# Performance work log

Hardware: AMD Instinct MI355X
Metric: run time of the kernel (lower is better)

The kernel has to match this reference:

```python
import jax, jax.numpy as jnp
import numpy as np

T = 35            # cfg.VOXEL_POINT_COUNT
D, H, W = 10, 400, 352  # cfg.INPUT_DEPTH/HEIGHT/WIDTH
EPS = 1e-5


def _vfe(x, mask, w, b, gamma, beta):
    # x: [K, T, Cin]; mask: [K, T, 1]
    h = jax.nn.relu(jnp.einsum('ktc,cu->ktu', x, w) + b)        # [K, T, U]
    mean = jnp.mean(h, axis=(0, 1))
    var = jnp.var(h, axis=(0, 1))
    h = (h - mean) * jax.lax.rsqrt(var + EPS) * gamma + beta    # batch-stat BN
    agg = jnp.max(h, axis=1, keepdims=True)                     # [K, 1, U]
    cat = jnp.concatenate([h, jnp.broadcast_to(agg, h.shape)], axis=-1)  # [K, T, 2U]
    return cat * mask


def setup_inputs() -> dict:
    key = jax.random.key(0)
    ks = jax.random.split(key, 12)
    K = 40000
    feature = jax.random.normal(ks[0], (K, T, 7), dtype=jnp.float32)
    # zero out ~half the points so the nonzero mask is meaningful
    keep = jax.random.bernoulli(ks[1], 0.5, (K, T, 1)).astype(jnp.float32)
    feature = feature * keep
    bidx = jax.random.randint(ks[2], (K, 1), 0, 2)
    didx = jax.random.randint(ks[3], (K, 1), 0, D)
    hidx = jax.random.randint(ks[4], (K, 1), 0, H)
    widx = jax.random.randint(ks[5], (K, 1), 0, W)
    coordinate = jnp.concatenate([bidx, didx, hidx, widx], axis=1).astype(jnp.int32)
    s = 0.1
    return {
        'feature': feature,
        'w1': jax.random.normal(ks[6], (7, 16), dtype=jnp.float32) * s,
        'b1': jnp.zeros((16,), dtype=jnp.float32),
        'gamma1': jnp.ones((16,), dtype=jnp.float32),
        'beta1': jnp.zeros((16,), dtype=jnp.float32),
        'w2': jax.random.normal(ks[7], (32, 32), dtype=jnp.float32) * s,
        'b2': jnp.zeros((32,), dtype=jnp.float32),
        'gamma2': jnp.ones((32,), dtype=jnp.float32),
        'beta2': jnp.zeros((32,), dtype=jnp.float32),
        'coordinate': coordinate,
        'batch_size': 2,
    }


def reference(feature, w1, b1, gamma1, beta1, w2, b2, gamma2, beta2, coordinate, batch_size):
    # mask: voxel point is valid if any channel nonzero (max over channels != 0)
    mask = (jnp.max(feature, axis=2, keepdims=True) != 0).astype(feature.dtype)  # [K, T, 1]
    x = _vfe(feature, mask, w1, b1, gamma1, beta1)   # [K, T, 32]
    x = _vfe(x, mask, w2, b2, gamma2, beta2)         # [K, T, 64]
    voxelwise = jnp.max(x, axis=1)                   # [K, 64]
    out = jnp.zeros((batch_size, D, H, W, 64), dtype=voxelwise.dtype)
    out = out.at[coordinate[:, 0], coordinate[:, 1], coordinate[:, 2], coordinate[:, 3]].add(voxelwise)
    return out
```

## Files before the change

kernel.cpp:

```cpp
#include <hip/hip_runtime.h>
#include <math.h>

#define TT 35
#define DD 10
#define HD 400
#define WD 352
#define CIN 7
#define U1 16
#define U2 32
#define EPSV 1e-5f

#define WS_A1 0
#define WS_B1 16
#define WS_A2 32
#define WS_B2 64
#define WS_SUM1 256
#define WS_SSQ1 768
#define WS_SUM2 1280
#define WS_SSQ2 3328
#define NC1 32
#define NC2 64
#define WS_ZERO_FLOATS 5376

__global__ __launch_bounds__(256) void k_stats1(
    const float* __restrict__ feat, const float* __restrict__ w1,
    const float* __restrict__ b1, float* __restrict__ ws, int P) {
  __shared__ float s_w1[CIN * U1];
  __shared__ float s_b1[U1];
  __shared__ float s_red[4][2 * U1];

  int tid = threadIdx.x;
  if (tid < CIN * U1) s_w1[tid] = w1[tid];
  if (tid < U1) s_b1[tid] = b1[tid];
  __syncthreads();

  float sum[U1], ssq[U1];
#pragma unroll
  for (int u = 0; u < U1; ++u) { sum[u] = 0.f; ssq[u] = 0.f; }

  int stride = gridDim.x * blockDim.x;
  for (int p = blockIdx.x * blockDim.x + tid; p < P; p += stride) {
    const float* f = feat + (size_t)p * CIN;
    float x[CIN];
#pragma unroll
    for (int c = 0; c < CIN; ++c) x[c] = f[c];
#pragma unroll
    for (int u = 0; u < U1; ++u) {
      float acc = s_b1[u];
#pragma unroll
      for (int c = 0; c < CIN; ++c) acc += x[c] * s_w1[c * U1 + u];
      float h = fmaxf(acc, 0.f);
      sum[u] += h;
      ssq[u] += h * h;
    }
  }

  int lane = tid & 63, wv = tid >> 6;
#pragma unroll
  for (int u = 0; u < U1; ++u) {
    float s = sum[u], q = ssq[u];
    for (int off = 32; off; off >>= 1) {
      s += __shfl_down(s, off);
      q += __shfl_down(q, off);
    }
    if (lane == 0) { s_red[wv][u] = s; s_red[wv][U1 + u] = q; }
  }
  __syncthreads();
  if (tid < 2 * U1) {
    float tot = s_red[0][tid] + s_red[1][tid] + s_red[2][tid] + s_red[3][tid];
    int copy = blockIdx.x & (NC1 - 1);
    int u = tid & (U1 - 1);
    int base = (tid < U1) ? WS_SUM1 : WS_SSQ1;
    atomicAdd(&ws[base + copy * U1 + u], tot);
  }
}

__global__ void k_fin1(const float* __restrict__ gamma,
                       const float* __restrict__ beta, float* __restrict__ ws,
                       float invN) {
  int u = threadIdx.x;
  float s = 0.f, q = 0.f;
  for (int c = 0; c < NC1; ++c) {
    s += ws[WS_SUM1 + c * U1 + u];
    q += ws[WS_SSQ1 + c * U1 + u];
  }
  float mean = s * invN;
  float var = q * invN - mean * mean;
  float istd = 1.0f / sqrtf(var + EPSV);
  float A = gamma[u] * istd;
  ws[WS_A1 + u] = A;
  ws[WS_B1 + u] = beta[u] - mean * A;
}

__global__ void k_fin2(const float* __restrict__ gamma,
                       const float* __restrict__ beta, float* __restrict__ ws,
                       float invN) {
  int u = threadIdx.x;
  float s = 0.f, q = 0.f;
  for (int c = 0; c < NC2; ++c) {
    s += ws[WS_SUM2 + c * U2 + u];
    q += ws[WS_SSQ2 + c * U2 + u];
  }
  float mean = s * invN;
  float var = q * invN - mean * mean;
  float istd = 1.0f / sqrtf(var + EPSV);
  float A = gamma[u] * istd;
  ws[WS_A2 + u] = A;
  ws[WS_B2 + u] = beta[u] - mean * A;
}

template <bool FINAL>
__global__ __launch_bounds__(256) void k_vfe(
    const float* __restrict__ feat, const float* __restrict__ w1,
    const float* __restrict__ b1, const float* __restrict__ w2,
    const float* __restrict__ b2, const int* __restrict__ coord,
    float* __restrict__ ws, float* __restrict__ out, int K) {
  __shared__ float s_w1t[U1][9];
  __shared__ __align__(16) float s_w2t[U2 * U2];
  __shared__ float s_b1[U1], s_A1[U1], s_B1[U1];
  __shared__ float s_b2[U2], s_A2[U2], s_B2[U2];
  __shared__ float s_feat[4][TT * 9];
  __shared__ __align__(16) float s_cat[4][TT][U2];
  __shared__ float s_agg[4][U1];
  __shared__ float s_red[4][2 * U2];
  __shared__ __align__(16) float s_h2[FINAL ? 4 : 1][TT][U2];

  int tid = threadIdx.x;
  int lane = tid & 63, wv = tid >> 6;
  int v = blockIdx.x * 4 + wv;
  bool active = (v < K);

  if (tid < CIN * U1) {
    int u = tid / CIN, c = tid % CIN;
    s_w1t[u][c] = w1[c * U1 + u];
  }
  for (int i = tid; i < U2 * U2; i += 256) {
    int u = i >> 5, c = i & 31;
    s_w2t[i] = w2[c * U2 + u];
  }
  if (tid < U1) {
    s_b1[tid] = b1[tid];
    s_A1[tid] = ws[WS_A1 + tid];
    s_B1[tid] = ws[WS_B1 + tid];
  }
  if (tid < U2) {
    s_b2[tid] = b2[tid];
    s_A2[tid] = ws[WS_A2 + tid];
    s_B2[tid] = ws[WS_B2 + tid];
  }
  __syncthreads();

  if (active) {
    const float* fv = feat + (size_t)v * TT * CIN;
    for (int i = lane; i < TT * CIN; i += 64) {
      int t = i / CIN, c = i % CIN;
      s_feat[wv][t * 9 + c] = fv[i];
    }
  }
  __syncthreads();
  if (active && lane < TT) {
    float m = s_feat[wv][lane * 9 + 0];
#pragma unroll
    for (int c = 1; c < CIN; ++c) m = fmaxf(m, s_feat[wv][lane * 9 + c]);
    s_feat[wv][lane * 9 + 7] = (m != 0.f) ? 1.f : 0.f;
  }
  __syncthreads();

  if (active) {
    for (int i = lane; i < TT * U1; i += 64) {
      int t = i >> 4, u = i & 15;
      float acc = s_b1[u];
#pragma unroll
      for (int c = 0; c < CIN; ++c) acc += s_feat[wv][t * 9 + c] * s_w1t[u][c];
      float h = fmaxf(acc, 0.f);
      s_cat[wv][t][u] = s_A1[u] * h + s_B1[u];
    }
  }
  __syncthreads();
  if (active && lane < U1) {
    float m = s_cat[wv][0][lane];
    for (int t = 1; t < TT; ++t) m = fmaxf(m, s_cat[wv][t][lane]);
    s_agg[wv][lane] = m;
  }
  __syncthreads();
  if (active) {
    for (int i = lane; i < TT * U1; i += 64) {
      int t = i >> 4, u = i & 15;
      float mk = s_feat[wv][t * 9 + 7];
      s_cat[wv][t][u] *= mk;
      s_cat[wv][t][U1 + u] = s_agg[wv][u] * mk;
    }
  }
  __syncthreads();

  int u = lane & 31;
  int th = lane >> 5;
  float rw2[U2];
#pragma unroll
  for (int c4 = 0; c4 < 8; ++c4) {
    float4 v4 = *(const float4*)&s_w2t[u * U2 + 4 * c4];
    rw2[4 * c4 + 0] = v4.x;
    rw2[4 * c4 + 1] = v4.y;
    rw2[4 * c4 + 2] = v4.z;
    rw2[4 * c4 + 3] = v4.w;
  }
  float b2u = s_b2[u], A2u = s_A2[u], B2u = s_B2[u];
  float sum2 = 0.f, ssq2 = 0.f;
  if (active) {
    for (int t = th; t < TT; t += 2) {
      float acc = b2u;
      const float4* cr = (const float4*)&s_cat[wv][t][0];
#pragma unroll
      for (int c4 = 0; c4 < 8; ++c4) {
        float4 v4 = cr[c4];
        acc += v4.x * rw2[4 * c4] + v4.y * rw2[4 * c4 + 1] +
               v4.z * rw2[4 * c4 + 2] + v4.w * rw2[4 * c4 + 3];
      }
      float h = fmaxf(acc, 0.f);
      if (FINAL) {
        s_h2[wv][t][u] = A2u * h + B2u;
      } else {
        sum2 += h;
        ssq2 += h * h;
      }
    }
  }

  if (!FINAL) {
    float o1 = __shfl_down(sum2, 32);
    float o2 = __shfl_down(ssq2, 32);
    if (lane < 32) {
      s_red[wv][lane] = sum2 + o1;
      s_red[wv][U2 + lane] = ssq2 + o2;
    }
    __syncthreads();
    if (tid < 2 * U2) {
      float tot = s_red[0][tid] + s_red[1][tid] + s_red[2][tid] + s_red[3][tid];
      int copy = blockIdx.x & (NC2 - 1);
      int ch = tid & (U2 - 1);
      int base = (tid < U2) ? WS_SUM2 : WS_SSQ2;
      atomicAdd(&ws[base + copy * U2 + ch], tot);
    }
  } else {
    __syncthreads();
    float aggv = 0.f;
    if (active && lane < U2) {
      float m = s_h2[wv][0][lane];
      for (int t = 1; t < TT; ++t) m = fmaxf(m, s_h2[wv][t][lane]);
      aggv = m;
    }
    float aggb = __shfl(aggv, lane & 31);
    if (active) {
      int c = lane;
      float vox = -INFINITY;
      for (int t = 0; t < TT; ++t) {
        float mk = s_feat[wv][t * 9 + 7];
        float val = (c < U2) ? s_h2[wv][t][c] : aggb;
        vox = fmaxf(vox, val * mk);
      }
      const int4 cd = *(const int4*)&coord[4 * v];
      long base =
          ((((long)cd.x * DD + cd.y) * HD + cd.z) * WD + cd.w) * 64;
      atomicAdd(&out[base + c], vox);
    }
  }
}

extern "C" void kernel_launch(void* const* d_in, const int* in_sizes, int n_in,
                              void* d_out, int out_size, void* d_ws,
                              size_t ws_size, hipStream_t stream) {
  const float* feat = (const float*)d_in[0];
  const float* w1 = (const float*)d_in[1];
  const float* b1 = (const float*)d_in[2];
  const float* g1 = (const float*)d_in[3];
  const float* be1 = (const float*)d_in[4];
  const float* w2 = (const float*)d_in[5];
  const float* b2 = (const float*)d_in[6];
  const float* g2 = (const float*)d_in[7];
  const float* be2 = (const float*)d_in[8];
  const int* coord = (const int*)d_in[9];
  float* out = (float*)d_out;
  float* ws = (float*)d_ws;

  int K = in_sizes[0] / (TT * CIN);
  int P = K * TT;
  float invN = 1.0f / (float)P;

  (void)hipMemsetAsync(d_out, 0, (size_t)out_size * sizeof(float), stream);
  (void)hipMemsetAsync(d_ws, 0, WS_ZERO_FLOATS * sizeof(float), stream);

  k_stats1<<<512, 256, 0, stream>>>(feat, w1, b1, ws, P);
  k_fin1<<<1, U1, 0, stream>>>(g1, be1, ws, invN);

  int vb = (K + 3) / 4;
  k_vfe<false><<<vb, 256, 0, stream>>>(feat, w1, b1, w2, b2, nullptr, ws,
                                       nullptr, K);
  k_fin2<<<1, U2, 0, stream>>>(g2, be2, ws, invN);
  k_vfe<true><<<vb, 256, 0, stream>>>(feat, w1, b1, w2, b2, coord, ws, out, K);
}
```

Baseline: 1.023 ms.

## Use bf16 MFMA for VFE2, cache h2 in workspace, fuse finalizers and zeroing

```diff
diff --git a/kernel.cpp b/kernel.cpp
--- a/kernel.cpp
+++ b/kernel.cpp
@@ -10,17 +10,28 @@
 #define U2 32
 #define EPSV 1e-5f
 
-#define WS_A1 0
-#define WS_B1 16
-#define WS_A2 32
-#define WS_B2 64
 #define WS_SUM1 256
 #define WS_SSQ1 768
 #define WS_SUM2 1280
-#define WS_SSQ2 3328
+#define WS_SSQ2 1792
 #define NC1 32
-#define NC2 64
-#define WS_ZERO_FLOATS 5376
+#define NC2 16
+#define WS_ZERO_FLOATS 2304
+#define WS_H2_OFF_FLOATS 4096
+#define MASK_STRIDE 36
+
+typedef __bf16 bf16x8 __attribute__((ext_vector_type(8)));
+typedef float f32x4 __attribute__((ext_vector_type(4)));
+
+__device__ inline float bf2f(unsigned short b) {
+  unsigned u = ((unsigned)b) << 16;
+  return __builtin_bit_cast(float, u);
+}
+__device__ inline unsigned short f2bf(float x) {
+  unsigned u = __builtin_bit_cast(unsigned, x);
+  unsigned r = (u + 0x7fff + ((u >> 16) & 1)) >> 16;
+  return (unsigned short)r;
+}
 
 __global__ __launch_bounds__(256) void k_stats1(
     const float* __restrict__ feat, const float* __restrict__ w1,
@@ -75,195 +86,241 @@
   }
 }
 
-__global__ void k_fin1(const float* __restrict__ gamma,
-                       const float* __restrict__ beta, float* __restrict__ ws,
-                       float invN) {
-  int u = threadIdx.x;
-  float s = 0.f, q = 0.f;
-  for (int c = 0; c < NC1; ++c) {
-    s += ws[WS_SUM1 + c * U1 + u];
-    q += ws[WS_SSQ1 + c * U1 + u];
-  }
-  float mean = s * invN;
-  float var = q * invN - mean * mean;
-  float istd = 1.0f / sqrtf(var + EPSV);
-  float A = gamma[u] * istd;
-  ws[WS_A1 + u] = A;
-  ws[WS_B1 + u] = beta[u] - mean * A;
-}
-
-__global__ void k_fin2(const float* __restrict__ gamma,
-                       const float* __restrict__ beta, float* __restrict__ ws,
-                       float invN) {
-  int u = threadIdx.x;
-  float s = 0.f, q = 0.f;
-  for (int c = 0; c < NC2; ++c) {
-    s += ws[WS_SUM2 + c * U2 + u];
-    q += ws[WS_SSQ2 + c * U2 + u];
-  }
-  float mean = s * invN;
-  float var = q * invN - mean * mean;
-  float istd = 1.0f / sqrtf(var + EPSV);
-  float A = gamma[u] * istd;
-  ws[WS_A2 + u] = A;
-  ws[WS_B2 + u] = beta[u] - mean * A;
-}
-
-template <bool FINAL>
-__global__ __launch_bounds__(256) void k_vfe(
+__global__ __launch_bounds__(256) void k_vfe2(
     const float* __restrict__ feat, const float* __restrict__ w1,
-    const float* __restrict__ b1, const float* __restrict__ w2,
-    const float* __restrict__ b2, const int* __restrict__ coord,
-    float* __restrict__ ws, float* __restrict__ out, int K) {
-  __shared__ float s_w1t[U1][9];
-  __shared__ __align__(16) float s_w2t[U2 * U2];
-  __shared__ float s_b1[U1], s_A1[U1], s_B1[U1];
-  __shared__ float s_b2[U2], s_A2[U2], s_B2[U2];
-  __shared__ float s_feat[4][TT * 9];
-  __shared__ __align__(16) float s_cat[4][TT][U2];
-  __shared__ float s_agg[4][U1];
-  __shared__ float s_red[4][2 * U2];
-  __shared__ __align__(16) float s_h2[FINAL ? 4 : 1][TT][U2];
+    const float* __restrict__ b1, const float* __restrict__ g1,
+    const float* __restrict__ be1, const float* __restrict__ w2,
+    const float* __restrict__ b2, float* __restrict__ ws,
+    unsigned short* __restrict__ h2g, float* __restrict__ maskg,
+    float4* __restrict__ out4, long n4, int K, float invN) {
+  __shared__ unsigned short s_w2b[32 * 40];
+  __shared__ unsigned short s_catb[4][48][32];
+  __shared__ float s_red[4][64];
 
   int tid = threadIdx.x;
   int lane = tid & 63, wv = tid >> 6;
+  int g = lane >> 4, u = lane & 15;
   int v = blockIdx.x * 4 + wv;
   bool active = (v < K);
 
-  if (tid < CIN * U1) {
-    int u = tid / CIN, c = tid % CIN;
-    s_w1t[u][c] = w1[c * U1 + u];
-  }
-  for (int i = tid; i < U2 * U2; i += 256) {
-    int u = i >> 5, c = i & 31;
-    s_w2t[i] = w2[c * U2 + u];
-  }
-  if (tid < U1) {
-    s_b1[tid] = b1[tid];
-    s_A1[tid] = ws[WS_A1 + tid];
-    s_B1[tid] = ws[WS_B1 + tid];
-  }
-  if (tid < U2) {
-    s_b2[tid] = b2[tid];
-    s_A2[tid] = ws[WS_A2 + tid];
-    s_B2[tid] = ws[WS_B2 + tid];
+  for (int i = tid; i < 32 * 32; i += 256) {
+    int n = i >> 5, cp = i & 31;
+    int c = (cp & 1) ? (16 + (cp >> 1)) : (cp >> 1);
+    s_w2b[n * 40 + cp] = f2bf(w2[c * 32 + n]);
+  }
+  {
+    unsigned* z = (unsigned*)s_catb;
+    for (int i = tid; i < 4 * 13 * 16; i += 256) {
+      int w = i / 208, rem = i % 208;
+      int row = 35 + (rem >> 4), k = rem & 15;
+      z[(w * 48 + row) * 16 + k] = 0u;
+    }
+  }
+
+  float s1 = 0.f, q1 = 0.f;
+#pragma unroll
+  for (int c = 0; c < NC1; ++c) {
+    s1 += ws[WS_SUM1 + c * U1 + u];
+    q1 += ws[WS_SSQ1 + c * U1 + u];
+  }
+  float mean1 = s1 * invN;
+  float var1 = q1 * invN - mean1 * mean1;
+  float A1 = g1[u] / sqrtf(var1 + EPSV);
+  float B1 = be1[u] - mean1 * A1;
+
+  float w1r[CIN];
+#pragma unroll
+  for (int c = 0; c < CIN; ++c) w1r[c] = w1[c * U1 + u];
+  float b1u = b1[u];
+
+  float h1n[9], mkv[9];
+  float aggl = -INFINITY;
+  const float* fv = feat + (size_t)v * (TT * CIN);
+#pragma unroll
+  for (int j = 0; j < 9; ++j) {
+    int t = g + 4 * j;
+    h1n[j] = -INFINITY;
+    mkv[j] = 0.f;
+    if (active && t < TT) {
+      const float* fr = fv + t * CIN;
+      float x0 = fr[0], x1 = fr[1], x2 = fr[2], x3 = fr[3];
+      float x4 = fr[4], x5 = fr[5], x6 = fr[6];
+      float m = fmaxf(fmaxf(fmaxf(x0, x1), fmaxf(x2, x3)),
+                      fmaxf(fmaxf(x4, x5), x6));
+      float mk = (m != 0.f) ? 1.f : 0.f;
+      float acc = b1u + x0 * w1r[0] + x1 * w1r[1] + x2 * w1r[2] +
+                  x3 * w1r[3] + x4 * w1r[4] + x5 * w1r[5] + x6 * w1r[6];
+      float h = fmaxf(acc, 0.f);
+      h1n[j] = A1 * h + B1;
+      mkv[j] = mk;
+      if (u == 0) maskg[(size_t)v * MASK_STRIDE + t] = mk;
+      aggl = fmaxf(aggl, h1n[j]);
+    }
+  }
+  aggl = fmaxf(aggl, __shfl_xor(aggl, 16));
+  aggl = fmaxf(aggl, __shfl_xor(aggl, 32));
+
+#pragma unroll
+  for (int j = 0; j < 9; ++j) {
+    int t = g + 4 * j;
+    if (active && t < TT) {
+      unsigned pk = (unsigned)f2bf(h1n[j] * mkv[j]) |
+                    ((unsigned)f2bf(aggl * mkv[j]) << 16);
+      *(unsigned*)&s_catb[wv][t][2 * u] = pk;
+    }
   }
   __syncthreads();
 
+  f32x4 acc[2][3];
+#pragma unroll
+  for (int nt = 0; nt < 2; ++nt)
+#pragma unroll
+    for (int mt = 0; mt < 3; ++mt) acc[nt][mt] = (f32x4)(0.f);
+
+  bf16x8 bfr[2];
+#pragma unroll
+  for (int nt = 0; nt < 2; ++nt) {
+    uint4 raw = *(const uint4*)&s_w2b[(nt * 16 + u) * 40 + g * 8];
+    bfr[nt] = __builtin_bit_cast(bf16x8, raw);
+  }
+#pragma unroll
+  for (int mt = 0; mt < 3; ++mt) {
+    uint4 raw = *(const uint4*)&s_catb[wv][mt * 16 + u][g * 8];
+    bf16x8 afr = __builtin_bit_cast(bf16x8, raw);
+#pragma unroll
+    for (int nt = 0; nt < 2; ++nt)
+      acc[nt][mt] =
+          __builtin_amdgcn_mfma_f32_16x16x32_bf16(afr, bfr[nt], acc[nt][mt], 0, 0, 0);
+  }
+
+  float b2c[2] = {b2[u], b2[16 + u]};
+  float sum[2] = {0.f, 0.f}, ssq[2] = {0.f, 0.f};
+#pragma unroll
+  for (int nt = 0; nt < 2; ++nt) {
+#pragma unroll
+    for (int mt = 0; mt < 3; ++mt) {
+      unsigned pk[2];
+      float hv[4];
+#pragma unroll
+      for (int r = 0; r < 4; ++r) {
+        int row = mt * 16 + g * 4 + r;
+        float h = fmaxf(acc[nt][mt][r] + b2c[nt], 0.f);
+        hv[r] = h;
+        if (row < TT) {
+          sum[nt] += h;
+          ssq[nt] += h * h;
+        }
+      }
+      pk[0] = (unsigned)f2bf(hv[0]) | ((unsigned)f2bf(hv[1]) << 16);
+      pk[1] = (unsigned)f2bf(hv[2]) | ((unsigned)f2bf(hv[3]) << 16);
+      if (active) {
+        uint2 st = make_uint2(pk[0], pk[1]);
+        *(uint2*)&h2g[((size_t)v * 6 + nt * 3 + mt) * 256 + lane * 4] = st;
+      }
+    }
+  }
+
+#pragma unroll
+  for (int nt = 0; nt < 2; ++nt) {
+    sum[nt] += __shfl_xor(sum[nt], 16);
+    sum[nt] += __shfl_xor(sum[nt], 32);
+    ssq[nt] += __shfl_xor(ssq[nt], 16);
+    ssq[nt] += __shfl_xor(ssq[nt], 32);
+  }
+  float contrib = 0.f;
   if (active) {
-    const float* fv = feat + (size_t)v * TT * CIN;
-    for (int i = lane; i < TT * CIN; i += 64) {
-      int t = i / CIN, c = i % CIN;
-      s_feat[wv][t * 9 + c] = fv[i];
-    }
-  }
+    contrib = (g == 0) ? sum[0] : (g == 1) ? sum[1] : (g == 2) ? ssq[0] : ssq[1];
+  }
+  s_red[wv][(g & 1) * 16 + u + (g >> 1) * 32] = contrib;
   __syncthreads();
-  if (active && lane < TT) {
-    float m = s_feat[wv][lane * 9 + 0];
-#pragma unroll
-    for (int c = 1; c < CIN; ++c) m = fmaxf(m, s_feat[wv][lane * 9 + c]);
-    s_feat[wv][lane * 9 + 7] = (m != 0.f) ? 1.f : 0.f;
-  }
-  __syncthreads();
-
-  if (active) {
-    for (int i = lane; i < TT * U1; i += 64) {
-      int t = i >> 4, u = i & 15;
-      float acc = s_b1[u];
-#pragma unroll
-      for (int c = 0; c < CIN; ++c) acc += s_feat[wv][t * 9 + c] * s_w1t[u][c];
-      float h = fmaxf(acc, 0.f);
-      s_cat[wv][t][u] = s_A1[u] * h + s_B1[u];
-    }
-  }
-  __syncthreads();
-  if (active && lane < U1) {
-    float m = s_cat[wv][0][lane];
-    for (int t = 1; t < TT; ++t) m = fmaxf(m, s_cat[wv][t][lane]);
-    s_agg[wv][lane] = m;
-  }
-  __syncthreads();
-  if (active) {
-    for (int i = lane; i < TT * U1; i += 64) {
-      int t = i >> 4, u = i & 15;
-      float mk = s_feat[wv][t * 9 + 7];
-      s_cat[wv][t][u] *= mk;
-      s_cat[wv][t][U1 + u] = s_agg[wv][u] * mk;
-    }
-  }
-  __syncthreads();
-
-  int u = lane & 31;
-  int th = lane >> 5;
-  float rw2[U2];
-#pragma unroll
-  for (int c4 = 0; c4 < 8; ++c4) {
-    float4 v4 = *(const float4*)&s_w2t[u * U2 + 4 * c4];
-    rw2[4 * c4 + 0] = v4.x;
-    rw2[4 * c4 + 1] = v4.y;
-    rw2[4 * c4 + 2] = v4.z;
-    rw2[4 * c4 + 3] = v4.w;
-  }
-  float b2u = s_b2[u], A2u = s_A2[u], B2u = s_B2[u];
-  float sum2 = 0.f, ssq2 = 0.f;
-  if (active) {
-    for (int t = th; t < TT; t += 2) {
-      float acc = b2u;
-      const float4* cr = (const float4*)&s_cat[wv][t][0];
-#pragma unroll
-      for (int c4 = 0; c4 < 8; ++c4) {
-        float4 v4 = cr[c4];
-        acc += v4.x * rw2[4 * c4] + v4.y * rw2[4 * c4 + 1] +
-               v4.z * rw2[4 * c4 + 2] + v4.w * rw2[4 * c4 + 3];
+  if (tid < 64) {
+    float tot = s_red[0][tid] + s_red[1][tid] + s_red[2][tid] + s_red[3][tid];
+    int copy = blockIdx.x & (NC2 - 1);
+    int ch = tid & 31;
+    int base = (tid < 32) ? WS_SUM2 : WS_SSQ2;
+    atomicAdd(&ws[base + copy * U2 + ch], tot);
+  }
+
+  long gtid = (long)blockIdx.x * 256 + tid;
+  long gstride = (long)gridDim.x * 256;
+  float4 zz = make_float4(0.f, 0.f, 0.f, 0.f);
+  for (long i = gtid; i < n4; i += gstride) out4[i] = zz;
+}
+
+__global__ __launch_bounds__(256) void k_final(
+    const unsigned short* __restrict__ h2g, const float* __restrict__ maskg,
+    const float* __restrict__ ws, const float* __restrict__ g2,
+    const float* __restrict__ be2, const int* __restrict__ coord,
+    float* __restrict__ out, int K, float invN) {
+  int tid = threadIdx.x;
+  int lane = tid & 63, wv = tid >> 6;
+  int g = lane >> 4, u = lane & 15;
+  int v = blockIdx.x * 4 + wv;
+  if (v >= K) return;
+
+  float A2[2], B2[2];
+#pragma unroll
+  for (int h = 0; h < 2; ++h) {
+    int ch = h * 16 + u;
+    float s = 0.f, q = 0.f;
+#pragma unroll
+    for (int c = 0; c < NC2; ++c) {
+      s += ws[WS_SUM2 + c * U2 + ch];
+      q += ws[WS_SSQ2 + c * U2 + ch];
+    }
+    float mean = s * invN;
+    float var = q * invN - mean * mean;
+    float A = g2[ch] / sqrtf(var + EPSV);
+    A2[h] = A;
+    B2[h] = be2[ch] - mean * A;
+  }
+
+  float vox[2] = {-INFINITY, -INFINITY};
+  float agg[2] = {-INFINITY, -INFINITY};
+  float cnt = 0.f;
+#pragma unroll
+  for (int mt = 0; mt < 3; ++mt) {
+    const float4 mk4 = *(const float4*)&maskg[(size_t)v * MASK_STRIDE + mt * 16 + g * 4];
+    float mk[4] = {mk4.x, mk4.y, mk4.z, mk4.w};
+#pragma unroll
+    for (int nt = 0; nt < 2; ++nt) {
+      uint2 raw = *(const uint2*)&h2g[((size_t)v * 6 + nt * 3 + mt) * 256 + lane * 4];
+      unsigned short e[4] = {(unsigned short)(raw.x & 0xffff),
+                             (unsigned short)(raw.x >> 16),
+                             (unsigned short)(raw.y & 0xffff),
+                             (unsigned short)(raw.y >> 16)};
+#pragma unroll
+      for (int r = 0; r < 4; ++r) {
+        int row = mt * 16 + g * 4 + r;
+        if (row < TT) {
+          float hn = A2[nt] * bf2f(e[r]) + B2[nt];
+          agg[nt] = fmaxf(agg[nt], hn);
+          vox[nt] = fmaxf(vox[nt], hn * mk[r]);
+          if (nt == 0) cnt += mk[r];
+        }
       }
-      float h = fmaxf(acc, 0.f);
-      if (FINAL) {
-        s_h2[wv][t][u] = A2u * h + B2u;
-      } else {
-        sum2 += h;
-        ssq2 += h * h;
-      }
-    }
-  }
-
-  if (!FINAL) {
-    float o1 = __shfl_down(sum2, 32);
-    float o2 = __shfl_down(ssq2, 32);
-    if (lane < 32) {
-      s_red[wv][lane] = sum2 + o1;
-      s_red[wv][U2 + lane] = ssq2 + o2;
-    }
-    __syncthreads();
-    if (tid < 2 * U2) {
-      float tot = s_red[0][tid] + s_red[1][tid] + s_red[2][tid] + s_red[3][tid];
-      int copy = blockIdx.x & (NC2 - 1);
-      int ch = tid & (U2 - 1);
-      int base = (tid < U2) ? WS_SUM2 : WS_SSQ2;
-      atomicAdd(&ws[base + copy * U2 + ch], tot);
-    }
+    }
+  }
+#pragma unroll
+  for (int nt = 0; nt < 2; ++nt) {
+    vox[nt] = fmaxf(vox[nt], __shfl_xor(vox[nt], 16));
+    vox[nt] = fmaxf(vox[nt], __shfl_xor(vox[nt], 32));
+    agg[nt] = fmaxf(agg[nt], __shfl_xor(agg[nt], 16));
+    agg[nt] = fmaxf(agg[nt], __shfl_xor(agg[nt], 32));
+  }
+  cnt += __shfl_xor(cnt, 16);
+  cnt += __shfl_xor(cnt, 32);
+
+  float val;
+  if (lane < 32) {
+    val = (lane < 16) ? vox[0] : vox[1];
   } else {
-    __syncthreads();
-    float aggv = 0.f;
-    if (active && lane < U2) {
-      float m = s_h2[wv][0][lane];
-      for (int t = 1; t < TT; ++t) m = fmaxf(m, s_h2[wv][t][lane]);
-      aggv = m;
-    }
-    float aggb = __shfl(aggv, lane & 31);
-    if (active) {
-      int c = lane;
-      float vox = -INFINITY;
-      for (int t = 0; t < TT; ++t) {
-        float mk = s_feat[wv][t * 9 + 7];
-        float val = (c < U2) ? s_h2[wv][t][c] : aggb;
-        vox = fmaxf(vox, val * mk);
-      }
-      const int4 cd = *(const int4*)&coord[4 * v];
-      long base =
-          ((((long)cd.x * DD + cd.y) * HD + cd.z) * WD + cd.w) * 64;
-      atomicAdd(&out[base + c], vox);
-    }
-  }
+    float a = (lane < 48) ? agg[0] : agg[1];
+    val = (cnt > 0.5f) ? ((cnt < TT - 0.5f) ? fmaxf(a, 0.f) : a) : 0.f;
+  }
+  const int4 cd = *(const int4*)&coord[4 * v];
+  long base = ((((long)cd.x * DD + cd.y) * HD + cd.z) * WD + cd.w) * 64;
+  atomicAdd(&out[base + lane], val);
 }
 
 extern "C" void kernel_launch(void* const* d_in, const int* in_sizes, int n_in,
@@ -285,16 +342,17 @@
   int K = in_sizes[0] / (TT * CIN);
   int P = K * TT;
   float invN = 1.0f / (float)P;
-
-  (void)hipMemsetAsync(d_out, 0, (size_t)out_size * sizeof(float), stream);
+  long n4 = (long)out_size / 4;
+
+  unsigned short* h2g = (unsigned short*)(ws + WS_H2_OFF_FLOATS);
+  float* maskg = (float*)(h2g + (size_t)K * 6 * 256);
+
   (void)hipMemsetAsync(d_ws, 0, WS_ZERO_FLOATS * sizeof(float), stream);
 
   k_stats1<<<512, 256, 0, stream>>>(feat, w1, b1, ws, P);
-  k_fin1<<<1, U1, 0, stream>>>(g1, be1, ws, invN);
 
   int vb = (K + 3) / 4;
-  k_vfe<false><<<vb, 256, 0, stream>>>(feat, w1, b1, w2, b2, nullptr, ws,
-                                       nullptr, K);
-  k_fin2<<<1, U2, 0, stream>>>(g2, be2, ws, invN);
-  k_vfe<true><<<vb, 256, 0, stream>>>(feat, w1, b1, w2, b2, coord, ws, out, K);
-}
+  k_vfe2<<<vb, 256, 0, stream>>>(feat, w1, b1, g1, be1, w2, b2, ws, h2g, maskg,
+                                 (float4*)out, n4, K, invN);
+  k_final<<<vb, 256, 0, stream>>>(h2g, maskg, ws, g2, be2, coord, out, K, invN);
+}
```

New measurement: 911.3 us. 10.9% less time.
